# Kernel optimization log

Measured on AMD Instinct MI355X. Metric: run time of the kernel, lower is better.

The kernel has to match this reference:

```python
import jax, jax.numpy as jnp
import numpy as np
import math

B, S, D, H = 2, 2048, 1024, 16
DH = D // H
NEG = -1e9


def gelu(x):
    return 0.5 * x * (1.0 + jnp.tanh(math.sqrt(2.0 / math.pi) * (x + 0.044715 * x ** 3)))


def layernorm(x, g, b, eps=1e-6):
    # faithful to module: uses std (unbiased, N-1) and adds eps to std, not var
    mean = jnp.mean(x, axis=-1, keepdims=True)
    var = jnp.sum((x - mean) ** 2, axis=-1, keepdims=True) / (x.shape[-1] - 1)
    std = jnp.sqrt(var)
    return g * (x - mean) / (std + eps) + b


def setup_inputs() -> dict:
    key = jax.random.key(0)
    ks = jax.random.split(key, 13)
    sd = 0.02
    return {
        "x": jax.random.normal(ks[0], (B, S, D), jnp.float32),
        "w_attn": jax.random.normal(ks[1], (D, 3 * D), jnp.float32) * sd,
        "b_attn": jnp.zeros((3 * D,), jnp.float32),
        "w_aproj": jax.random.normal(ks[2], (D, D), jnp.float32) * sd,
        "b_aproj": jnp.zeros((D,), jnp.float32),
        "g1": jnp.ones((D,), jnp.float32),
        "b1": jnp.zeros((D,), jnp.float32),
        "w_fc": jax.random.normal(ks[3], (D, 4 * D), jnp.float32) * sd,
        "b_fc": jnp.zeros((4 * D,), jnp.float32),
        "w_mproj": jax.random.normal(ks[4], (4 * D, D), jnp.float32) * sd,
        "b_mproj": jnp.zeros((D,), jnp.float32),
        "g2": jnp.ones((D,), jnp.float32),
        "b2": jnp.zeros((D,), jnp.float32),
    }


def reference(x, w_attn, b_attn, w_aproj, b_aproj, g1, b1, w_fc, b_fc, w_mproj, b_mproj, g2, b2):
    # --- attention ---
    qkv = x @ w_attn + b_attn                       # [B,S,3D]
    q, k, v = jnp.split(qkv, 3, axis=2)
    q = q.reshape(B, S, H, DH).transpose(0, 2, 1, 3)  # [B,H,S,DH]
    k = k.reshape(B, S, H, DH).transpose(0, 2, 1, 3)
    v = v.reshape(B, S, H, DH).transpose(0, 2, 1, 3)
    w = jnp.einsum('bhqd,bhkd->bhqk', q, k) / math.sqrt(DH)
    mask = jnp.tril(jnp.ones((S, S), jnp.float32))[None, None]
    w = w * mask + NEG * (1.0 - mask)
    w = jax.nn.softmax(w, axis=-1)
    a = jnp.einsum('bhqk,bhkd->bhqd', w, v)         # [B,H,S,DH]
    a = a.transpose(0, 2, 1, 3).reshape(B, S, D)
    a = a @ w_aproj + b_aproj
    # --- postLN + MLP ---
    n = layernorm(x + a, g1, b1)
    h = gelu(n @ w_fc + b_fc)
    m = h @ w_mproj + b_mproj
    return layernorm(n + m, g2, b2)
```

## Files before the change

kernel.cpp:

```cpp
#include <hip/hip_runtime.h>
#include <type_traits>


typedef unsigned short u16;
typedef short s16x8 __attribute__((ext_vector_type(8)));
typedef unsigned short u16x4 __attribute__((ext_vector_type(4)));
typedef float f32x4 __attribute__((ext_vector_type(4)));
typedef float f32x16 __attribute__((ext_vector_type(16)));

__device__ __forceinline__ u16 f2b(float f) {
    union { float f; unsigned u; } x{f};
    unsigned r = x.u + 0x7FFFu + ((x.u >> 16) & 1u);
    return (u16)(r >> 16);
}

__device__ __forceinline__ f32x4 mfma16(s16x8 a, s16x8 b, f32x4 c) {
    return __builtin_amdgcn_mfma_f32_16x16x32_bf16(a, b, c, 0, 0, 0);
}

__device__ __forceinline__ f32x16 mfma32(s16x8 a, s16x8 b, f32x16 c) {
    return __builtin_amdgcn_mfma_f32_32x32x16_bf16(a, b, c, 0, 0, 0);
}

__device__ __forceinline__ int cvtpk(float a, float b) {
    int r;
    asm("v_cvt_pk_bf16_f32 %0, %1, %2" : "=v"(r) : "v"(a), "v"(b));
    return r;
}

__device__ __forceinline__ void gld_lds16(const u16* g, u16* l) {
    __builtin_amdgcn_global_load_lds(
        (const __attribute__((address_space(1))) void*)g,
        (__attribute__((address_space(3))) void*)l, 16, 0, 0);
}

__global__ __launch_bounds__(256) void cvt_bf16(const float* __restrict__ in,
                                                u16* __restrict__ out, int n4) {
    int i = blockIdx.x * 256 + threadIdx.x;
    if (i < n4) {
        float4 v = ((const float4*)in)[i];
        u16x4 o = {f2b(v.x), f2b(v.y), f2b(v.z), f2b(v.w)};
        ((u16x4*)out)[i] = o;
    }
}

__global__ __launch_bounds__(256) void transpose_bf16(const float* __restrict__ W,
                                                      u16* __restrict__ WT,
                                                      int K, int N) {
    __shared__ float t[32][33];
    int tx = threadIdx.x & 31, ty = threadIdx.x >> 5;
    int n0 = blockIdx.x * 32, k0 = blockIdx.y * 32;
    #pragma unroll
    for (int r = ty; r < 32; r += 8)
        t[r][tx] = W[(size_t)(k0 + r) * N + n0 + tx];
    __syncthreads();
    #pragma unroll
    for (int r = ty; r < 32; r += 8)
        WT[(size_t)(n0 + r) * K + k0 + tx] = f2b(t[tx][r]);
}

template<int BN, bool GELU, typename OT>
__global__ __launch_bounds__(256) void gemm_db(const u16* __restrict__ A,
                                               const u16* __restrict__ BT,
                                               const float* __restrict__ bias,
                                               OT* __restrict__ C,
                                               int M, int N, int K, int ldc) {
    constexpr int NF = BN / 32;
    constexpr int BNI = BN / 32;
    __shared__ u16 As[2][128 * 64];
    __shared__ u16 Bs[2][BN * 64];

    int t = threadIdx.x;
    int w = t >> 6, l = t & 63, l16 = l & 15, lh = l >> 4;
    int wr = w >> 1, wc = w & 1;

    int nbm = M >> 7;
    int cpx = gridDim.x >> 3;
    int id = blockIdx.x;
    int id2 = (id & 7) * cpx + (id >> 3);
    size_t m0 = (size_t)(id2 % nbm) * 128;
    size_t n0 = (size_t)(id2 / nbm) * BN;

    int rowA = t >> 3;
    int gc = t & 7;
    int gc2 = gc ^ (((rowA >> 2) & 1) << 1) ^ (((rowA >> 3) & 1) << 2);
    const u16* Ag = A + (m0 + rowA) * (size_t)K + gc2 * 8;
    const u16* Bg = BT + (n0 + rowA) * (size_t)K + gc2 * 8;
    int wbase = w * 512;

    f32x4 acc[4][NF] = {};
    int cxor = (((l16 >> 2) & 1) << 4) ^ (((l16 >> 3) & 1) << 5);

    #pragma unroll
    for (int j = 0; j < 4; ++j)
        gld_lds16(Ag + (size_t)j * 32 * K, &As[0][j * 2048 + wbase]);
    #pragma unroll
    for (int j = 0; j < BNI; ++j)
        gld_lds16(Bg + (size_t)j * 32 * K, &Bs[0][j * 2048 + wbase]);
    __syncthreads();

    int cur = 0;
    for (int k0 = 0; k0 < K; k0 += 64) {
        if (k0 + 64 < K) {
            const u16* Ap = Ag + k0 + 64;
            #pragma unroll
            for (int j = 0; j < 4; ++j)
                gld_lds16(Ap + (size_t)j * 32 * K, &As[cur ^ 1][j * 2048 + wbase]);
            const u16* Bp = Bg + k0 + 64;
            #pragma unroll
            for (int j = 0; j < BNI; ++j)
                gld_lds16(Bp + (size_t)j * 32 * K, &Bs[cur ^ 1][j * 2048 + wbase]);
        }
        __builtin_amdgcn_s_setprio(1);
        #pragma unroll
        for (int ks = 0; ks < 2; ++ks) {
            s16x8 af[4], bf[NF];
            #pragma unroll
            for (int fm = 0; fm < 4; ++fm) {
                int row = wr * 64 + fm * 16 + l16;
                int col = (ks * 32 + lh * 8) ^ cxor;
                af[fm] = *(const s16x8*)&As[cur][row * 64 + col];
            }
            #pragma unroll
            for (int fn = 0; fn < NF; ++fn) {
                int row = wc * (BN / 2) + fn * 16 + l16;
                int col = (ks * 32 + lh * 8) ^ cxor;
                bf[fn] = *(const s16x8*)&Bs[cur][row * 64 + col];
            }
            #pragma unroll
            for (int fm = 0; fm < 4; ++fm)
                #pragma unroll
                for (int fn = 0; fn < NF; ++fn)
                    acc[fm][fn] = mfma16(af[fm], bf[fn], acc[fm][fn]);
        }
        __builtin_amdgcn_s_setprio(0);
        __syncthreads();
        cur ^= 1;
    }

    #pragma unroll
    for (int fn = 0; fn < NF; ++fn) {
        size_t col = n0 + wc * (BN / 2) + fn * 16 + l16;
        float bs = bias[col];
        #pragma unroll
        for (int fm = 0; fm < 4; ++fm) {
            size_t row0 = m0 + wr * 64 + fm * 16 + lh * 4;
            #pragma unroll
            for (int i = 0; i < 4; ++i) {
                float v = acc[fm][fn][i] + bs;
                if constexpr (GELU) {
                    float x3 = v * v * v;
                    v = 0.5f * v * (1.f + tanhf(0.7978845608f * (v + 0.044715f * x3)));
                }
                if constexpr (std::is_same<OT, u16>::value)
                    C[(row0 + i) * ldc + col] = f2b(v);
                else
                    C[(row0 + i) * ldc + col] = v;
            }
        }
    }
}

__global__ __launch_bounds__(256, 1) void attn_kernel(const u16* __restrict__ qkv,
                                                      u16* __restrict__ abuf) {
    constexpr int S = 2048, D3 = 3072, Dm = 1024;
    __shared__ u16 Kl[2][64 * 64];
    __shared__ u16 Vt[2][64 * 64];

    int t = threadIdx.x;
    int w = t >> 6, l = t & 63;
    int l32 = l & 31, hi = l >> 5;
    int pr = blockIdx.x >> 5;
    int bh = blockIdx.x & 31;
    int b = bh >> 4, h = bh & 15;
    size_t base = (size_t)b * S * D3;

    int rK0 = t >> 3, gK = t & 7;
    int rK1 = rK0 + 32;
    size_t koff0 = (size_t)rK0 * D3 + (size_t)((gK ^ (rK0 & 7)) * 8);
    size_t koff1 = (size_t)rK1 * D3 + (size_t)((gK ^ (rK1 & 7)) * 8);
    const u16* kbase = qkv + base + Dm + h * 64;
    const u16* vbase = qkv + base + 2 * Dm + h * 64 + w * 16;

    constexpr float cexp = 0.18033688011112042f;
    constexpr float THR = 64.0f;
    int xg = l32 & 7;

    #pragma unroll 1
    for (int ph = 0; ph < 2; ++ph) {
        int qt = ph ? (15 - pr) : pr;
        int qb = qt * 128 + w * 32;
        int nst = 2 * (qt + 1);

        s16x8 qf[4];
        const u16* qp = qkv + base + (size_t)(qb + l32) * D3 + h * 64 + hi * 8;
        #pragma unroll
        for (int kk = 0; kk < 4; ++kk)
            qf[kk] = *(const s16x8*)(qp + kk * 16);

        f32x16 O0 = {}, O1 = {};
        float m = -1e30f, lr = 0.f;

        gld_lds16(kbase + koff0, &Kl[0][w * 512]);
        gld_lds16(kbase + koff1, &Kl[0][2048 + w * 512]);
        {
            const u16* vp = vbase + (size_t)l * D3;
            s16x8 pv0 = *(const s16x8*)vp;
            s16x8 pv1 = *(const s16x8*)(vp + 8);
            #pragma unroll
            for (int e = 0; e < 8; ++e) {
                int d0 = w * 16 + e, d1 = w * 16 + 8 + e;
                Vt[0][d0 * 64 + (l ^ ((d0 & 7) << 3))] = (u16)pv0[e];
                Vt[0][d1 * 64 + (l ^ ((d1 & 7) << 3))] = (u16)pv1[e];
            }
        }
        __syncthreads();

        #pragma unroll 1
        for (int sc = 0; sc < nst; ++sc) {
            int cur = sc & 1;
            bool pre = (sc + 1 < nst);
            s16x8 v0, v1;
            if (pre) {
                size_t koffc = (size_t)(sc + 1) * 64 * D3;
                gld_lds16(kbase + koffc + koff0, &Kl[cur ^ 1][w * 512]);
                gld_lds16(kbase + koffc + koff1, &Kl[cur ^ 1][2048 + w * 512]);
                const u16* vp = vbase + (size_t)((sc + 1) * 64 + l) * D3;
                v0 = *(const s16x8*)vp;
                v1 = *(const s16x8*)(vp + 8);
            }

            int kvb = sc * 64;
            int navail = ((qb - kvb) >> 5) + 1;
            if (navail > 0) {
                if (navail > 2) navail = 2;
                const u16* Kc = Kl[cur];
                const u16* Vc = Vt[cur];
                f32x16 sa0 = {}, sa1 = {};
                #pragma unroll
                for (int kk = 0; kk < 4; ++kk) {
                    s16x8 kf = *(const s16x8*)&Kc[l32 * 64 + (((2 * kk + hi) ^ xg) * 8)];
                    sa0 = mfma32(kf, qf[kk], sa0);
                }
                if (navail == 2) {
                    #pragma unroll
                    for (int kk = 0; kk < 4; ++kk) {
                        s16x8 kf = *(const s16x8*)&Kc[(32 + l32) * 64 + (((2 * kk + hi) ^ xg) * 8)];
                        sa1 = mfma32(kf, qf[kk], sa1);
                    }
                }
                bool diag0 = (kvb == qb);
                bool diag1 = (kvb + 32 == qb);
                float p[32];
                float mx = -1e30f;
                #pragma unroll
                for (int reg = 0; reg < 16; ++reg) {
                    int kvloc = (reg & 3) + 8 * (reg >> 2) + 4 * hi;
                    float s0 = sa0[reg];
                    if (diag0 && kvloc > l32) s0 = -1e30f;
                    p[reg] = s0;
                    mx = fmaxf(mx, s0);
                }
                if (navail == 2) {
                    #pragma unroll
                    for (int reg = 0; reg < 16; ++reg) {
                        int kvloc = (reg & 3) + 8 * (reg >> 2) + 4 * hi;
                        float s1 = sa1[reg];
                        if (diag1 && kvloc > l32) s1 = -1e30f;
                        p[16 + reg] = s1;
                        mx = fmaxf(mx, s1);
                    }
                }
                mx = fmaxf(mx, __shfl_xor(mx, 32));
                if (!__all(mx <= m + THR)) {
                    float mn = fmaxf(m, mx);
                    float a_ = exp2f(cexp * (m - mn));
                    m = mn;
                    #pragma unroll
                    for (int reg = 0; reg < 16; ++reg) {
                        int src = (reg & 3) + 8 * (reg >> 2) + 4 * hi;
                        float aq = __shfl(a_, src);
                        O0[reg] *= aq;
                        O1[reg] *= aq;
                    }
                    lr *= a_;
                }
                float rs = 0.f;
                #pragma unroll
                for (int reg = 0; reg < 16; ++reg) {
                    p[reg] = exp2f(cexp * (p[reg] - m));
                    rs += p[reg];
                }
                if (navail == 2) {
                    #pragma unroll
                    for (int reg = 16; reg < 32; ++reg) {
                        p[reg] = exp2f(cexp * (p[reg] - m));
                        rs += p[reg];
                    }
                }
                rs += __shfl_xor(rs, 32);
                lr += rs;

                #pragma unroll
                for (int c = 0; c < 4; ++c) {
                    if (c < navail * 2) {
                        int pb = (c >> 1) * 16 + (c & 1) * 8;
                        int pk01 = cvtpk(p[pb + 0], p[pb + 1]);
                        int pk23 = cvtpk(p[pb + 2], p[pb + 3]);
                        int pk45 = cvtpk(p[pb + 4], p[pb + 5]);
                        int pk67 = cvtpk(p[pb + 6], p[pb + 7]);
                        int sx01 = __shfl_xor(pk01, 32);
                        int sx23 = __shfl_xor(pk23, 32);
                        int sx45 = __shfl_xor(pk45, 32);
                        int sx67 = __shfl_xor(pk67, 32);
                        union { int i[4]; s16x8 v; } u;
                        u.i[0] = hi ? sx45 : pk01;
                        u.i[1] = hi ? sx67 : pk23;
                        u.i[2] = hi ? pk45 : sx01;
                        u.i[3] = hi ? pk67 : sx23;
                        int go = ((c * 2 + hi) ^ xg) * 8;
                        s16x8 vb0 = *(const s16x8*)&Vc[l32 * 64 + go];
                        O0 = mfma32(u.v, vb0, O0);
                        s16x8 vb1 = *(const s16x8*)&Vc[(32 + l32) * 64 + go];
                        O1 = mfma32(u.v, vb1, O1);
                    }
                }
            }

            if (pre) {
                #pragma unroll
                for (int e = 0; e < 8; ++e) {
                    int d0 = w * 16 + e, d1 = w * 16 + 8 + e;
                    Vt[cur ^ 1][d0 * 64 + (l ^ ((d0 & 7) << 3))] = (u16)v0[e];
                    Vt[cur ^ 1][d1 * 64 + (l ^ ((d1 & 7) << 3))] = (u16)v1[e];
                }
            }
            __syncthreads();
        }

        float invl = 1.f / lr;
        size_t obase = (size_t)b * S * 1024 + h * 64;
        #pragma unroll
        for (int reg = 0; reg < 16; ++reg) {
            int src = (reg & 3) + 8 * (reg >> 2) + 4 * hi;
            float iq = __shfl(invl, src);
            size_t row = obase + (size_t)(qb + src) * 1024;
            abuf[row + l32] = f2b(O0[reg] * iq);
            abuf[row + 32 + l32] = f2b(O1[reg] * iq);
        }
    }
}

template<bool WB>
__global__ __launch_bounds__(256) void resln(const float* __restrict__ xa,
                                             const float* __restrict__ xb2,
                                             const float* __restrict__ g,
                                             const float* __restrict__ be,
                                             float* __restrict__ outf,
                                             u16* __restrict__ outb) {
    int row = blockIdx.x;
    int t = threadIdx.x;
    size_t base = (size_t)row * 1024 + t * 4;
    float4 va = *(const float4*)(xa + base);
    float4 vb = *(const float4*)(xb2 + base);
    float v0 = va.x + vb.x, v1 = va.y + vb.y, v2 = va.z + vb.z, v3 = va.w + vb.w;
    float s1 = v0 + v1 + v2 + v3;
    float s2 = v0 * v0 + v1 * v1 + v2 * v2 + v3 * v3;
    #pragma unroll
    for (int off = 32; off >= 1; off >>= 1) {
        s1 += __shfl_down(s1, off);
        s2 += __shfl_down(s2, off);
    }
    __shared__ float r1[4], r2[4];
    if ((t & 63) == 0) { r1[t >> 6] = s1; r2[t >> 6] = s2; }
    __syncthreads();
    s1 = r1[0] + r1[1] + r1[2] + r1[3];
    s2 = r2[0] + r2[1] + r2[2] + r2[3];
    float mean = s1 * (1.f / 1024.f);
    float var = fmaxf((s2 - 1024.f * mean * mean) * (1.f / 1023.f), 0.f);
    float inv = 1.f / (sqrtf(var) + 1e-6f);
    int col = t * 4;
    float y0 = g[col + 0] * ((v0 - mean) * inv) + be[col + 0];
    float y1 = g[col + 1] * ((v1 - mean) * inv) + be[col + 1];
    float y2 = g[col + 2] * ((v2 - mean) * inv) + be[col + 2];
    float y3 = g[col + 3] * ((v3 - mean) * inv) + be[col + 3];
    float4 o = {y0, y1, y2, y3};
    *(float4*)(outf + base) = o;
    if constexpr (WB) {
        u16x4 ob = {f2b(y0), f2b(y1), f2b(y2), f2b(y3)};
        *(u16x4*)(outb + base) = ob;
    }
}

extern "C" void kernel_launch(void* const* d_in, const int* in_sizes, int n_in,
                              void* d_out, int out_size, void* d_ws, size_t ws_size,
                              hipStream_t stream) {
    (void)in_sizes; (void)n_in; (void)out_size; (void)ws_size;
    const float* x       = (const float*)d_in[0];
    const float* w_attn  = (const float*)d_in[1];
    const float* b_attn  = (const float*)d_in[2];
    const float* w_aproj = (const float*)d_in[3];
    const float* b_aproj = (const float*)d_in[4];
    const float* g1      = (const float*)d_in[5];
    const float* b1      = (const float*)d_in[6];
    const float* w_fc    = (const float*)d_in[7];
    const float* b_fc    = (const float*)d_in[8];
    const float* w_mproj = (const float*)d_in[9];
    const float* b_mproj = (const float*)d_in[10];
    const float* g2      = (const float*)d_in[11];
    const float* b2      = (const float*)d_in[12];
    float* out = (float*)d_out;

    constexpr int M = 4096;
    constexpr int D = 1024;

    char* ws = (char*)d_ws;
    u16*   slotA = (u16*)ws;
    char*  pB    = ws + (32u << 20);
    char*  pC    = ws + (40u << 20);
    char*  pD    = ws + (48u << 20);
    char*  pE    = ws + (64u << 20);

    u16*   xb   = (u16*)pB;
    u16*   wT   = (u16*)pC;
    u16*   qkv  = slotA;
    u16*   abuf = (u16*)pB;
    float* aout = (float*)pD;
    float* nbuf = (float*)pE;
    u16*   nb   = (u16*)pB;
    u16*   h    = slotA;
    float* mout = (float*)pD;

    dim3 blk(256);

    cvt_bf16<<<dim3(4096), blk, 0, stream>>>(x, xb, M * D / 4);

    transpose_bf16<<<dim3(3072 / 32, 1024 / 32), blk, 0, stream>>>(w_attn, wT, 1024, 3072);
    gemm_db<128, false, u16><<<dim3((M / 128) * (3072 / 128)), blk, 0, stream>>>(
        xb, wT, b_attn, qkv, M, 3072, 1024, 3072);

    attn_kernel<<<dim3(256), blk, 0, stream>>>(qkv, abuf);

    transpose_bf16<<<dim3(1024 / 32, 1024 / 32), blk, 0, stream>>>(w_aproj, wT, 1024, 1024);
    gemm_db<64, false, float><<<dim3((M / 128) * (1024 / 64)), blk, 0, stream>>>(
        abuf, wT, b_aproj, aout, M, 1024, 1024, 1024);

    resln<true><<<dim3(M), blk, 0, stream>>>(x, aout, g1, b1, nbuf, nb);

    transpose_bf16<<<dim3(4096 / 32, 1024 / 32), blk, 0, stream>>>(w_fc, wT, 1024, 4096);
    gemm_db<128, true, u16><<<dim3((M / 128) * (4096 / 128)), blk, 0, stream>>>(
        nb, wT, b_fc, h, M, 4096, 1024, 4096);

    transpose_bf16<<<dim3(1024 / 32, 4096 / 32), blk, 0, stream>>>(w_mproj, wT, 4096, 1024);
    gemm_db<64, false, float><<<dim3((M / 128) * (1024 / 64)), blk, 0, stream>>>(
        h, wT, b_mproj, mout, M, 1024, 4096, 1024);

    resln<false><<<dim3(M), blk, 0, stream>>>(nbuf, mout, g2, b2, out, nullptr);
}
```

Measured before the change: 314.1 us.

## Split attention KV range three ways with a merge kernel (flash-decoding style)

The attention kernel now splits each query tile's KV chunk range into three parts, launching three times as many blocks. Each block writes an unnormalized bf16 partial output plus per-row (max, sum) stats, and a new merge kernel combines the three partials with rescaling. The aim is to fill more of the GPU's compute units, since the old grid had only 256 blocks. The cost is an extra kernel launch, extra global traffic for the partials and stats, and an extra bf16 rounding of the unnormalized partials. Launch bounds are relaxed from one block per unit.

```diff
diff --git a/kernel.cpp b/kernel.cpp
--- a/kernel.cpp
+++ b/kernel.cpp
@@ -12,6 +12,12 @@
     union { float f; unsigned u; } x{f};
     unsigned r = x.u + 0x7FFFu + ((x.u >> 16) & 1u);
     return (u16)(r >> 16);
+}
+
+__device__ __forceinline__ float b2f(u16 v) {
+    union { unsigned u; float f; } x;
+    x.u = ((unsigned)v) << 16;
+    return x.f;
 }
 
 __device__ __forceinline__ f32x4 mfma16(s16x8 a, s16x8 b, f32x4 c) {
@@ -161,8 +167,11 @@
     }
 }
 
-__global__ __launch_bounds__(256, 1) void attn_kernel(const u16* __restrict__ qkv,
-                                                      u16* __restrict__ abuf) {
+__global__ __launch_bounds__(256) void attn_kernel(const u16* __restrict__ qkv,
+                                                   u16* __restrict__ p0,
+                                                   u16* __restrict__ p1,
+                                                   u16* __restrict__ p2,
+                                                   float2* __restrict__ stats) {
     constexpr int S = 2048, D3 = 3072, Dm = 1024;
     __shared__ u16 Kl[2][64 * 64];
     __shared__ u16 Vt[2][64 * 64];
@@ -170,10 +179,14 @@
     int t = threadIdx.x;
     int w = t >> 6, l = t & 63;
     int l32 = l & 31, hi = l >> 5;
-    int pr = blockIdx.x >> 5;
-    int bh = blockIdx.x & 31;
+    int bid = blockIdx.x;
+    int bh = bid & 31;
+    int pr = (bid >> 5) & 7;
+    int third = bid >> 8;
     int b = bh >> 4, h = bh & 15;
     size_t base = (size_t)b * S * D3;
+
+    u16* pout = third == 0 ? p0 : (third == 1 ? p1 : p2);
 
     int rK0 = t >> 3, gK = t & 7;
     int rK1 = rK0 + 32;
@@ -191,164 +204,207 @@
         int qt = ph ? (15 - pr) : pr;
         int qb = qt * 128 + w * 32;
         int nst = 2 * (qt + 1);
-
-        s16x8 qf[4];
-        const u16* qp = qkv + base + (size_t)(qb + l32) * D3 + h * 64 + hi * 8;
-        #pragma unroll
-        for (int kk = 0; kk < 4; ++kk)
-            qf[kk] = *(const s16x8*)(qp + kk * 16);
+        int c0 = (nst * third) / 3;
+        int c1 = (nst * (third + 1)) / 3;
 
         f32x16 O0 = {}, O1 = {};
         float m = -1e30f, lr = 0.f;
 
-        gld_lds16(kbase + koff0, &Kl[0][w * 512]);
-        gld_lds16(kbase + koff1, &Kl[0][2048 + w * 512]);
-        {
-            const u16* vp = vbase + (size_t)l * D3;
-            s16x8 pv0 = *(const s16x8*)vp;
-            s16x8 pv1 = *(const s16x8*)(vp + 8);
-            #pragma unroll
-            for (int e = 0; e < 8; ++e) {
-                int d0 = w * 16 + e, d1 = w * 16 + 8 + e;
-                Vt[0][d0 * 64 + (l ^ ((d0 & 7) << 3))] = (u16)pv0[e];
-                Vt[0][d1 * 64 + (l ^ ((d1 & 7) << 3))] = (u16)pv1[e];
+        if (c0 < c1) {
+            s16x8 qf[4];
+            const u16* qp = qkv + base + (size_t)(qb + l32) * D3 + h * 64 + hi * 8;
+            #pragma unroll
+            for (int kk = 0; kk < 4; ++kk)
+                qf[kk] = *(const s16x8*)(qp + kk * 16);
+
+            size_t kc0 = (size_t)c0 * 64 * D3;
+            gld_lds16(kbase + kc0 + koff0, &Kl[0][w * 512]);
+            gld_lds16(kbase + kc0 + koff1, &Kl[0][2048 + w * 512]);
+            {
+                const u16* vp = vbase + (size_t)(c0 * 64 + l) * D3;
+                s16x8 pv0 = *(const s16x8*)vp;
+                s16x8 pv1 = *(const s16x8*)(vp + 8);
+                #pragma unroll
+                for (int e = 0; e < 8; ++e) {
+                    int d0 = w * 16 + e, d1 = w * 16 + 8 + e;
+                    Vt[0][d0 * 64 + (l ^ ((d0 & 7) << 3))] = (u16)pv0[e];
+                    Vt[0][d1 * 64 + (l ^ ((d1 & 7) << 3))] = (u16)pv1[e];
+                }
             }
-        }
-        __syncthreads();
-
-        #pragma unroll 1
-        for (int sc = 0; sc < nst; ++sc) {
-            int cur = sc & 1;
-            bool pre = (sc + 1 < nst);
-            s16x8 v0, v1;
-            if (pre) {
-                size_t koffc = (size_t)(sc + 1) * 64 * D3;
-                gld_lds16(kbase + koffc + koff0, &Kl[cur ^ 1][w * 512]);
-                gld_lds16(kbase + koffc + koff1, &Kl[cur ^ 1][2048 + w * 512]);
-                const u16* vp = vbase + (size_t)((sc + 1) * 64 + l) * D3;
-                v0 = *(const s16x8*)vp;
-                v1 = *(const s16x8*)(vp + 8);
-            }
-
-            int kvb = sc * 64;
-            int navail = ((qb - kvb) >> 5) + 1;
-            if (navail > 0) {
-                if (navail > 2) navail = 2;
-                const u16* Kc = Kl[cur];
-                const u16* Vc = Vt[cur];
-                f32x16 sa0 = {}, sa1 = {};
-                #pragma unroll
-                for (int kk = 0; kk < 4; ++kk) {
-                    s16x8 kf = *(const s16x8*)&Kc[l32 * 64 + (((2 * kk + hi) ^ xg) * 8)];
-                    sa0 = mfma32(kf, qf[kk], sa0);
+            __syncthreads();
+
+            #pragma unroll 1
+            for (int sc = c0; sc < c1; ++sc) {
+                int cur = (sc - c0) & 1;
+                bool pre = (sc + 1 < c1);
+                s16x8 v0, v1;
+                if (pre) {
+                    size_t koffc = (size_t)(sc + 1) * 64 * D3;
+                    gld_lds16(kbase + koffc + koff0, &Kl[cur ^ 1][w * 512]);
+                    gld_lds16(kbase + koffc + koff1, &Kl[cur ^ 1][2048 + w * 512]);
+                    const u16* vp = vbase + (size_t)((sc + 1) * 64 + l) * D3;
+                    v0 = *(const s16x8*)vp;
+                    v1 = *(const s16x8*)(vp + 8);
                 }
-                if (navail == 2) {
+
+                int kvb = sc * 64;
+                int navail = ((qb - kvb) >> 5) + 1;
+                if (navail > 0) {
+                    if (navail > 2) navail = 2;
+                    const u16* Kc = Kl[cur];
+                    const u16* Vc = Vt[cur];
+                    f32x16 sa0 = {}, sa1 = {};
                     #pragma unroll
                     for (int kk = 0; kk < 4; ++kk) {
-                        s16x8 kf = *(const s16x8*)&Kc[(32 + l32) * 64 + (((2 * kk + hi) ^ xg) * 8)];
-                        sa1 = mfma32(kf, qf[kk], sa1);
-                    }
-                }
-                bool diag0 = (kvb == qb);
-                bool diag1 = (kvb + 32 == qb);
-                float p[32];
-                float mx = -1e30f;
-                #pragma unroll
-                for (int reg = 0; reg < 16; ++reg) {
-                    int kvloc = (reg & 3) + 8 * (reg >> 2) + 4 * hi;
-                    float s0 = sa0[reg];
-                    if (diag0 && kvloc > l32) s0 = -1e30f;
-                    p[reg] = s0;
-                    mx = fmaxf(mx, s0);
-                }
-                if (navail == 2) {
+                        s16x8 kf = *(const s16x8*)&Kc[l32 * 64 + (((2 * kk + hi) ^ xg) * 8)];
+                        sa0 = mfma32(kf, qf[kk], sa0);
+                    }
+                    if (navail == 2) {
+                        #pragma unroll
+                        for (int kk = 0; kk < 4; ++kk) {
+                            s16x8 kf = *(const s16x8*)&Kc[(32 + l32) * 64 + (((2 * kk + hi) ^ xg) * 8)];
+                            sa1 = mfma32(kf, qf[kk], sa1);
+                        }
+                    }
+                    bool diag0 = (kvb == qb);
+                    bool diag1 = (kvb + 32 == qb);
+                    float p[32];
+                    float mx = -1e30f;
                     #pragma unroll
                     for (int reg = 0; reg < 16; ++reg) {
                         int kvloc = (reg & 3) + 8 * (reg >> 2) + 4 * hi;
-                        float s1 = sa1[reg];
-                        if (diag1 && kvloc > l32) s1 = -1e30f;
-                        p[16 + reg] = s1;
-                        mx = fmaxf(mx, s1);
-                    }
-                }
-                mx = fmaxf(mx, __shfl_xor(mx, 32));
-                if (!__all(mx <= m + THR)) {
-                    float mn = fmaxf(m, mx);
-                    float a_ = exp2f(cexp * (m - mn));
-                    m = mn;
+                        float s0 = sa0[reg];
+                        if (diag0 && kvloc > l32) s0 = -1e30f;
+                        p[reg] = s0;
+                        mx = fmaxf(mx, s0);
+                    }
+                    if (navail == 2) {
+                        #pragma unroll
+                        for (int reg = 0; reg < 16; ++reg) {
+                            int kvloc = (reg & 3) + 8 * (reg >> 2) + 4 * hi;
+                            float s1 = sa1[reg];
+                            if (diag1 && kvloc > l32) s1 = -1e30f;
+                            p[16 + reg] = s1;
+                            mx = fmaxf(mx, s1);
+                        }
+                    }
+                    mx = fmaxf(mx, __shfl_xor(mx, 32));
+                    if (!__all(mx <= m + THR)) {
+                        float mn = fmaxf(m, mx);
+                        float a_ = exp2f(cexp * (m - mn));
+                        m = mn;
+                        #pragma unroll
+                        for (int reg = 0; reg < 16; ++reg) {
+                            int src = (reg & 3) + 8 * (reg >> 2) + 4 * hi;
+                            float aq = __shfl(a_, src);
+                            O0[reg] *= aq;
+                            O1[reg] *= aq;
+                        }
+                        lr *= a_;
+                    }
+                    float rs = 0.f;
                     #pragma unroll
                     for (int reg = 0; reg < 16; ++reg) {
-                        int src = (reg & 3) + 8 * (reg >> 2) + 4 * hi;
-                        float aq = __shfl(a_, src);
-                        O0[reg] *= aq;
-                        O1[reg] *= aq;
-                    }
-                    lr *= a_;
-                }
-                float rs = 0.f;
-                #pragma unroll
-                for (int reg = 0; reg < 16; ++reg) {
-                    p[reg] = exp2f(cexp * (p[reg] - m));
-                    rs += p[reg];
-                }
-                if (navail == 2) {
-                    #pragma unroll
-                    for (int reg = 16; reg < 32; ++reg) {
                         p[reg] = exp2f(cexp * (p[reg] - m));
                         rs += p[reg];
                     }
+                    if (navail == 2) {
+                        #pragma unroll
+                        for (int reg = 16; reg < 32; ++reg) {
+                            p[reg] = exp2f(cexp * (p[reg] - m));
+                            rs += p[reg];
+                        }
+                    }
+                    rs += __shfl_xor(rs, 32);
+                    lr += rs;
+
+                    #pragma unroll
+                    for (int c = 0; c < 4; ++c) {
+                        if (c < navail * 2) {
+                            int pb = (c >> 1) * 16 + (c & 1) * 8;
+                            int pk01 = cvtpk(p[pb + 0], p[pb + 1]);
+                            int pk23 = cvtpk(p[pb + 2], p[pb + 3]);
+                            int pk45 = cvtpk(p[pb + 4], p[pb + 5]);
+                            int pk67 = cvtpk(p[pb + 6], p[pb + 7]);
+                            int sx01 = __shfl_xor(pk01, 32);
+                            int sx23 = __shfl_xor(pk23, 32);
+                            int sx45 = __shfl_xor(pk45, 32);
+                            int sx67 = __shfl_xor(pk67, 32);
+                            union { int i[4]; s16x8 v; } u;
+                            u.i[0] = hi ? sx45 : pk01;
+                            u.i[1] = hi ? sx67 : pk23;
+                            u.i[2] = hi ? pk45 : sx01;
+                            u.i[3] = hi ? pk67 : sx23;
+                            int go = ((c * 2 + hi) ^ xg) * 8;
+                            s16x8 vb0 = *(const s16x8*)&Vc[l32 * 64 + go];
+                            O0 = mfma32(u.v, vb0, O0);
+                            s16x8 vb1 = *(const s16x8*)&Vc[(32 + l32) * 64 + go];
+                            O1 = mfma32(u.v, vb1, O1);
+                        }
+                    }
                 }
-                rs += __shfl_xor(rs, 32);
-                lr += rs;
-
-                #pragma unroll
-                for (int c = 0; c < 4; ++c) {
-                    if (c < navail * 2) {
-                        int pb = (c >> 1) * 16 + (c & 1) * 8;
-                        int pk01 = cvtpk(p[pb + 0], p[pb + 1]);
-                        int pk23 = cvtpk(p[pb + 2], p[pb + 3]);
-                        int pk45 = cvtpk(p[pb + 4], p[pb + 5]);
-                        int pk67 = cvtpk(p[pb + 6], p[pb + 7]);
-                        int sx01 = __shfl_xor(pk01, 32);
-                        int sx23 = __shfl_xor(pk23, 32);
-                        int sx45 = __shfl_xor(pk45, 32);
-                        int sx67 = __shfl_xor(pk67, 32);
-                        union { int i[4]; s16x8 v; } u;
-                        u.i[0] = hi ? sx45 : pk01;
-                        u.i[1] = hi ? sx67 : pk23;
-                        u.i[2] = hi ? pk45 : sx01;
-                        u.i[3] = hi ? pk67 : sx23;
-                        int go = ((c * 2 + hi) ^ xg) * 8;
-                        s16x8 vb0 = *(const s16x8*)&Vc[l32 * 64 + go];
-                        O0 = mfma32(u.v, vb0, O0);
-                        s16x8 vb1 = *(const s16x8*)&Vc[(32 + l32) * 64 + go];
-                        O1 = mfma32(u.v, vb1, O1);
+
+                if (pre) {
+                    #pragma unroll
+                    for (int e = 0; e < 8; ++e) {
+                        int d0 = w * 16 + e, d1 = w * 16 + 8 + e;
+                        Vt[cur ^ 1][d0 * 64 + (l ^ ((d0 & 7) << 3))] = (u16)v0[e];
+                        Vt[cur ^ 1][d1 * 64 + (l ^ ((d1 & 7) << 3))] = (u16)v1[e];
                     }
                 }
+                __syncthreads();
             }
-
-            if (pre) {
-                #pragma unroll
-                for (int e = 0; e < 8; ++e) {
-                    int d0 = w * 16 + e, d1 = w * 16 + 8 + e;
-                    Vt[cur ^ 1][d0 * 64 + (l ^ ((d0 & 7) << 3))] = (u16)v0[e];
-                    Vt[cur ^ 1][d1 * 64 + (l ^ ((d1 & 7) << 3))] = (u16)v1[e];
-                }
-            }
-            __syncthreads();
         }
 
-        float invl = 1.f / lr;
         size_t obase = (size_t)b * S * 1024 + h * 64;
         #pragma unroll
         for (int reg = 0; reg < 16; ++reg) {
             int src = (reg & 3) + 8 * (reg >> 2) + 4 * hi;
-            float iq = __shfl(invl, src);
             size_t row = obase + (size_t)(qb + src) * 1024;
-            abuf[row + l32] = f2b(O0[reg] * iq);
-            abuf[row + 32 + l32] = f2b(O1[reg] * iq);
+            pout[row + l32] = f2b(O0[reg]);
+            pout[row + 32 + l32] = f2b(O1[reg]);
         }
-    }
+        if (hi == 0) {
+            float2 st; st.x = m; st.y = lr;
+            stats[third * 65536 + ((b * 2048 + qb + l32) * 16 + h)] = st;
+        }
+    }
+}
+
+__global__ __launch_bounds__(256) void merge_attn(u16* __restrict__ p0,
+                                                  const u16* __restrict__ p1,
+                                                  const u16* __restrict__ p2,
+                                                  const float2* __restrict__ stats) {
+    constexpr float cexp = 0.18033688011112042f;
+    int gid = blockIdx.x * 256 + threadIdx.x;
+    int rh = gid >> 2;
+    int dc = (gid & 3) * 16;
+    int R = rh >> 4, h = rh & 15;
+    size_t addr = (size_t)R * 1024 + h * 64 + dc;
+
+    float2 s0 = stats[rh];
+    float2 s1 = stats[65536 + rh];
+    float2 s2 = stats[131072 + rh];
+    float M = fmaxf(s0.x, fmaxf(s1.x, s2.x));
+    float a0 = exp2f(cexp * (s0.x - M));
+    float a1 = exp2f(cexp * (s1.x - M));
+    float a2 = exp2f(cexp * (s2.x - M));
+    float inv = 1.f / (a0 * s0.y + a1 * s1.y + a2 * s2.y);
+    a0 *= inv; a1 *= inv; a2 *= inv;
+
+    u16x4 o[4];
+    #pragma unroll
+    for (int j = 0; j < 4; ++j) {
+        u16x4 q0 = *(const u16x4*)(p0 + addr + j * 4);
+        u16x4 q1 = *(const u16x4*)(p1 + addr + j * 4);
+        u16x4 q2 = *(const u16x4*)(p2 + addr + j * 4);
+        #pragma unroll
+        for (int e = 0; e < 4; ++e)
+            o[j][e] = f2b(a0 * b2f(q0[e]) + a1 * b2f(q1[e]) + a2 * b2f(q2[e]));
+    }
+    #pragma unroll
+    for (int j = 0; j < 4; ++j)
+        *(u16x4*)(p0 + addr + j * 4) = o[j];
 }
 
 template<bool WB>
@@ -421,15 +477,19 @@
     char*  pD    = ws + (48u << 20);
     char*  pE    = ws + (64u << 20);
 
-    u16*   xb   = (u16*)pB;
-    u16*   wT   = (u16*)pC;
-    u16*   qkv  = slotA;
-    u16*   abuf = (u16*)pB;
-    float* aout = (float*)pD;
-    float* nbuf = (float*)pE;
-    u16*   nb   = (u16*)pB;
-    u16*   h    = slotA;
-    float* mout = (float*)pD;
+    u16*   xb    = (u16*)pB;
+    u16*   wT    = (u16*)pC;
+    u16*   qkv   = slotA;
+    u16*   part0 = (u16*)pB;
+    u16*   part1 = (u16*)pC;
+    u16*   part2 = (u16*)pD;
+    float2* stat = (float2*)pE;
+    u16*   abuf  = (u16*)pB;
+    float* aout  = (float*)pD;
+    float* nbuf  = (float*)pE;
+    u16*   nb    = (u16*)pB;
+    u16*   h     = slotA;
+    float* mout  = (float*)pD;
 
     dim3 blk(256);
 
@@ -439,7 +499,8 @@
     gemm_db<128, false, u16><<<dim3((M / 128) * (3072 / 128)), blk, 0, stream>>>(
         xb, wT, b_attn, qkv, M, 3072, 1024, 3072);
 
-    attn_kernel<<<dim3(256), blk, 0, stream>>>(qkv, abuf);
+    attn_kernel<<<dim3(768), blk, 0, stream>>>(qkv, part0, part1, part2, stat);
+    merge_attn<<<dim3(1024), blk, 0, stream>>>(part0, part1, part2, stat);
 
     transpose_bf16<<<dim3(1024 / 32, 1024 / 32), blk, 0, stream>>>(w_aproj, wT, 1024, 1024);
     gemm_db<64, false, float><<<dim3((M / 128) * (1024 / 64)), blk, 0, stream>>>(
```

Result: faster. 302.8 us (-3.6%).
